# Kernel tuning notes

Measured on AMD Instinct MI355X. Metric: run time of the kernel, lower is better.

## Reference

```python
import jax, jax.numpy as jnp
import numpy as np

B, T, NC, NB, D, DH = 128, 200, 3, 2, 512, 256
IMG_W, IMG_H = 640.0, 400.0


def setup_inputs() -> dict:
    key = jax.random.key(0)
    ks = jax.random.split(key, 16)
    # box_data: [x1,y1,x2,y2,category,confidence], some boxes zeroed (missing)
    coords = jax.random.uniform(ks[0], (B, T, NC * NB, 4)) * jnp.array([IMG_W, IMG_H, IMG_W, IMG_H])
    keep = (jax.random.uniform(ks[1], (B, T, NC * NB, 1)) > 0.2).astype(jnp.float32)
    coords = coords * keep
    cat = jax.random.randint(ks[2], (B, T, NC * NB, 1), 0, 3).astype(jnp.float32)
    conf = jax.random.uniform(ks[3], (B, T, NC * NB, 1))
    box_data = jnp.concatenate([coords, cat, conf], axis=-1)
    w = lambda k, shape: jax.random.normal(k, shape, jnp.float32) * 0.02
    return {
        "box_data": box_data,
        "cat_table": w(ks[4], (3, D)),
        "geom_w1": w(ks[5], (10, DH)), "geom_b1": jnp.zeros((DH,), jnp.float32),
        "ln_g": jnp.ones((DH,), jnp.float32), "ln_b": jnp.zeros((DH,), jnp.float32),
        "geom_w2": w(ks[6], (DH, D)), "geom_b2": jnp.zeros((D,), jnp.float32),
        "conf_w": w(ks[7], (1, D)), "conf_b": jnp.zeros((D,), jnp.float32),
        "center_w": w(ks[8], (2, D)), "center_b": jnp.zeros((D,), jnp.float32),
        "missing_emb": w(ks[9], (1, D)),
        "dist_w": w(ks[10], (1, D)), "dist_b": jnp.zeros((D,), jnp.float32),
        "cam_table": w(ks[11], (NC, D)),
        "scale": jnp.float32(3.0),
    }


def _layernorm(x, g, b, eps=1e-5):
    mu = jnp.mean(x, axis=-1, keepdims=True)
    var = jnp.mean(jnp.square(x - mu), axis=-1, keepdims=True)
    return (x - mu) * jax.lax.rsqrt(var + eps) * g + b


def reference(box_data, cat_table, geom_w1, geom_b1, ln_g, ln_b, geom_w2, geom_b2,
              conf_w, conf_b, center_w, center_b, missing_emb, dist_w, dist_b,
              cam_table, scale):
    coords = box_data[..., :4]                                 # (B,T,6,4)
    category = box_data[..., 4].astype(jnp.int32)
    conf = box_data[..., 5]
    norm = jnp.array([IMG_W, IMG_H, IMG_W, IMG_H], box_data.dtype)
    cn = (coords / norm).reshape(B, T, NC, NB, 4)              # normalized coords
    category = category.reshape(B, T, NC, NB)
    conf = conf.reshape(B, T, NC, NB, 1)
    presence = (cn.sum(-1) != 0).astype(box_data.dtype)        # (B,T,NC,NB)
    # sort boxes within each camera by category, missing boxes last
    sort_key = category.astype(box_data.dtype) + (1.0 - presence) * 1000.0
    idx = jnp.argsort(sort_key, axis=-1)                       # (B,T,NC,NB)
    cn = jnp.take_along_axis(cn, idx[..., None], axis=-2)
    category = jnp.take_along_axis(category, idx, axis=-1)
    conf = jnp.take_along_axis(conf, idx[..., None], axis=-2)
    presence = (cn.sum(-1) != 0).astype(box_data.dtype)[..., None]  # (B,T,NC,NB,1)

    x1, y1, x2, y2 = cn[..., 0], cn[..., 1], cn[..., 2], cn[..., 3]
    width, height = x2 - x1, y2 - y1
    cx, cy = (x1 + x2) * 0.5, (y1 + y2) * 0.5
    area = width * height
    aspect = width / (height + 1e-6)

    # distance token per camera (between the 2 boxes)
    dx, dy = cx[..., 0] - cx[..., 1], cy[..., 0] - cy[..., 1]
    dist = jnp.sqrt(dx * dx + dy * dy)[..., None]              # (B,T,NC,1)
    dist_tok = dist @ dist_w + dist_b                          # (B,T,NC,D)
    dist_flat = dist_tok.reshape(B, T * NC, D)

    geom = jnp.stack([x1, y1, x2, y2, width, height, cx, cy, area, aspect], axis=-1)
    h = _layernorm(geom @ geom_w1 + geom_b1, ln_g, ln_b)
    h = jax.nn.gelu(h, approximate=False)                      # torch GELU is exact
    geom_p = h @ geom_w2 + geom_b2                             # (B,T,NC,NB,D)

    cat_emb = cat_table[category]                              # (B,T,NC,NB,D)
    conf_p = conf @ conf_w + conf_b
    center_p = jnp.stack([cx, cy], axis=-1) @ center_w + center_b
    cam_emb = cam_table.reshape(1, 1, NC, 1, D)

    tok = (geom_p + cat_emb + conf_p + center_p + cam_emb) * scale
    tok = jnp.where(presence == 0, missing_emb, tok)           # (1,D) broadcasts
    tok_flat = tok.reshape(B, T * NC * NB, D)
    return jnp.concatenate([dist_flat, tok_flat], axis=1)      # (B, T*NC*(1+NB), D)
```

## Files before the change

### kernel.cpp

```cpp
#include <hip/hip_runtime.h>
#include <hip/hip_bf16.h>
#include <cstdint>

constexpr int Bn = 128, Tn = 200, NCn = 3, NBn = 2, Dn = 512, DHn = 256;
constexpr int GROUPS = Bn * Tn * NCn;
constexpr int TOKS   = GROUPS * NBn;

typedef __bf16 bf16x8 __attribute__((ext_vector_type(8)));
typedef float  f32x4  __attribute__((ext_vector_type(4)));

__device__ __forceinline__ unsigned short f2b(float f) {
    union { float f; unsigned int u; } x; x.f = f;
    unsigned int r = x.u + 0x7fffu + ((x.u >> 16) & 1u);
    return (unsigned short)(r >> 16);
}

__device__ __forceinline__ f32x4 ld4(const float* __restrict__ p) {
    return *reinterpret_cast<const f32x4*>(p);
}

__global__ __launch_bounds__(256) void k_tr(const float* __restrict__ w2,
                                            unsigned short* __restrict__ w2t) {
    int idx = blockIdx.x * 256 + threadIdx.x;
    int n = idx >> 8, k = idx & 255;
    w2t[idx] = f2b(w2[k * Dn + n]);
}

__global__ __launch_bounds__(256) void k_main(
    const float* __restrict__ bd,
    const float* __restrict__ cat_table,
    const float* __restrict__ w1,
    const float* __restrict__ b1,
    const float* __restrict__ ln_g,
    const float* __restrict__ ln_b,
    const float* __restrict__ b2v,
    const float* __restrict__ conf_w,
    const float* __restrict__ conf_b,
    const float* __restrict__ center_w,
    const float* __restrict__ center_b,
    const float* __restrict__ missing,
    const float* __restrict__ cam_table,
    const float* __restrict__ scale_p,
    const float* __restrict__ dist_w,
    const float* __restrict__ dist_b,
    const unsigned short* __restrict__ w2t,
    float* __restrict__ out) {

    __shared__ float s_geom[64][12];
    __shared__ float s_scal[64][4];
    __shared__ unsigned short s_a[64 * 264];

    const int tid = threadIdx.x;
    const int tb  = blockIdx.x * 64;

    if (tid < 32) {
        int g = blockIdx.x * 32 + tid;
        const float* p = bd + (size_t)g * 12;
        float v[12];
        #pragma unroll
        for (int i = 0; i < 12; i++) v[i] = p[i];
        float cn[2][4];
        cn[0][0] = v[0] / 640.f; cn[0][1] = v[1] / 400.f; cn[0][2] = v[2] / 640.f; cn[0][3] = v[3] / 400.f;
        cn[1][0] = v[6] / 640.f; cn[1][1] = v[7] / 400.f; cn[1][2] = v[8] / 640.f; cn[1][3] = v[9] / 400.f;
        float catv[2] = { v[4], v[10] };
        float cnfv[2] = { v[5], v[11] };
        float sum0 = cn[0][0] + cn[0][1] + cn[0][2] + cn[0][3];
        float sum1 = cn[1][0] + cn[1][1] + cn[1][2] + cn[1][3];
        float pr0 = (sum0 != 0.f) ? 1.f : 0.f;
        float pr1 = (sum1 != 0.f) ? 1.f : 0.f;
        float key0 = catv[0] + (1.f - pr0) * 1000.f;
        float key1 = catv[1] + (1.f - pr1) * 1000.f;
        int sw = (key1 < key0) ? 1 : 0;
        #pragma unroll
        for (int s = 0; s < 2; s++) {
            int src = s ^ sw;
            float x1 = cn[src][0], y1 = cn[src][1], x2 = cn[src][2], y2 = cn[src][3];
            float wd = x2 - x1, ht = y2 - y1;
            float cx = (x1 + x2) * 0.5f, cy = (y1 + y2) * 0.5f;
            float area = wd * ht, asp = wd / (ht + 1e-6f);
            float pres = ((x1 + y1 + x2 + y2) != 0.f) ? 1.f : 0.f;
            int lt = tid * 2 + s;
            s_geom[lt][0] = x1; s_geom[lt][1] = y1; s_geom[lt][2] = x2; s_geom[lt][3] = y2;
            s_geom[lt][4] = wd; s_geom[lt][5] = ht; s_geom[lt][6] = cx; s_geom[lt][7] = cy;
            s_geom[lt][8] = area; s_geom[lt][9] = asp; s_geom[lt][10] = 0.f; s_geom[lt][11] = 0.f;
            s_scal[lt][0] = cnfv[src]; s_scal[lt][1] = cx; s_scal[lt][2] = cy;
            s_scal[lt][3] = catv[src] + ((pres == 0.f) ? 4.f : 0.f);
        }
    }
    __syncthreads();

    const int w = tid >> 6, lane = tid & 63;

    {
        const int c0 = lane * 4;
        f32x4 w1r[10], b1r, gr, br;
        #pragma unroll
        for (int f = 0; f < 10; f++) w1r[f] = ld4(w1 + f * DHn + c0);
        b1r = ld4(b1 + c0); gr = ld4(ln_g + c0); br = ld4(ln_b + c0);
        for (int i = 0; i < 16; i++) {
            int lt = w * 16 + i;
            float gm[10];
            #pragma unroll
            for (int f = 0; f < 10; f++) gm[f] = s_geom[lt][f];
            float x[4];
            #pragma unroll
            for (int qq = 0; qq < 4; qq++) {
                float a = b1r[qq];
                #pragma unroll
                for (int f = 0; f < 10; f++) a += gm[f] * w1r[f][qq];
                x[qq] = a;
            }
            float s  = x[0] + x[1] + x[2] + x[3];
            float s2 = x[0]*x[0] + x[1]*x[1] + x[2]*x[2] + x[3]*x[3];
            #pragma unroll
            for (int m = 1; m < 64; m <<= 1) {
                s  += __shfl_xor(s,  m, 64);
                s2 += __shfl_xor(s2, m, 64);
            }
            float mu  = s * (1.f / 256.f);
            float var = s2 * (1.f / 256.f) - mu * mu;
            float rstd = rsqrtf(var + 1e-5f);
            ushort4 pk;
            #pragma unroll
            for (int qq = 0; qq < 4; qq++) {
                float t = (x[qq] - mu) * rstd * gr[qq] + br[qq];
                float y = 0.5f * t * (1.f + erff(t * 0.70710678118f));
                ((unsigned short*)&pk)[qq] = f2b(y);
            }
            *reinterpret_cast<ushort4*>(&s_a[lt * 264 + c0]) = pk;
        }
    }
    __syncthreads();

    const int mtp = w & 1;
    const int nh  = w >> 1;
    const int r16 = lane & 15, q = lane >> 4;

    bf16x8 afr[2][8];
    #pragma unroll
    for (int mt = 0; mt < 2; mt++) {
        int row = (mtp * 2 + mt) * 16 + r16;
        const unsigned short* base = &s_a[row * 264 + q * 8];
        #pragma unroll
        for (int ks = 0; ks < 8; ks++)
            afr[mt][ks] = *reinterpret_cast<const bf16x8*>(base + ks * 32);
    }

    float rconf[8], rcx[8], rcy[8];
    int rcat[8], rcam[8];
    size_t rowoff[8];
    bool rpres[8];
    #pragma unroll
    for (int i = 0; i < 8; i++) {
        int mt = i >> 2, r = i & 3;
        int m = (mtp * 2 + mt) * 16 + q * 4 + r;
        rconf[i] = s_scal[m][0]; rcx[i] = s_scal[m][1]; rcy[i] = s_scal[m][2];
        int code = (int)s_scal[m][3];
        rcat[i] = code & 3; rpres[i] = (code < 4);
        int gt = tb + m;
        rcam[i] = (gt >> 1) % 3;
        int b = gt / 1200, rr = gt - b * 1200;
        rowoff[i] = ((size_t)b * 1800 + 600 + rr) * Dn;
    }
    float sc = scale_p[0];

    for (int ntl = 0; ntl < 16; ntl++) {
        int n = (nh * 16 + ntl) * 16 + r16;
        float cb  = b2v[n] + conf_b[n] + center_b[n];
        float cwv = conf_w[n];
        float c0v = center_w[n];
        float c1v = center_w[Dn + n];
        float msv = missing[n];

        f32x4 acc0 = {0.f, 0.f, 0.f, 0.f}, acc1 = {0.f, 0.f, 0.f, 0.f};
        const unsigned short* bbase = w2t + n * 256 + q * 8;
        #pragma unroll
        for (int ks = 0; ks < 8; ks++) {
            bf16x8 bf = *reinterpret_cast<const bf16x8*>(bbase + ks * 32);
            acc0 = __builtin_amdgcn_mfma_f32_16x16x32_bf16(afr[0][ks], bf, acc0, 0, 0, 0);
            acc1 = __builtin_amdgcn_mfma_f32_16x16x32_bf16(afr[1][ks], bf, acc1, 0, 0, 0);
        }
        #pragma unroll
        for (int i = 0; i < 8; i++) {
            int mt = i >> 2, r = i & 3;
            float a = (mt == 0) ? acc0[r] : acc1[r];
            float ce = cat_table[rcat[i] * Dn + n];
            float cm = cam_table[rcam[i] * Dn + n];
            float v = (a + cb + ce + rconf[i] * cwv + rcx[i] * c0v + rcy[i] * c1v + cm) * sc;
            if (!rpres[i]) v = msv;
            out[rowoff[i] + n] = v;
        }
    }

    {
        const int gl2 = tid >> 7;
        const int col = (tid & 127) * 4;
        const f32x4 dwv = ld4(dist_w + col);
        const f32x4 dbv = ld4(dist_b + col);
        const int gblk = blockIdx.x * 32;
        for (int p = 0; p < 16; ++p) {
            int gl = p * 2 + gl2;
            float dx = s_scal[2 * gl][1] - s_scal[2 * gl + 1][1];
            float dy = s_scal[2 * gl][2] - s_scal[2 * gl + 1][2];
            float dist = sqrtf(dx * dx + dy * dy);
            int g = gblk + gl;
            int b = g / 600, r = g - b * 600;
            size_t ro = ((size_t)b * 1800 + r) * Dn + col;
            f32x4 v;
            #pragma unroll
            for (int r4 = 0; r4 < 4; r4++) v[r4] = dist * dwv[r4] + dbv[r4];
            *reinterpret_cast<f32x4*>(out + ro) = v;
        }
    }
}

extern "C" void kernel_launch(void* const* d_in, const int* in_sizes, int n_in,
                              void* d_out, int out_size, void* d_ws, size_t ws_size,
                              hipStream_t stream) {
    const float* bd        = (const float*)d_in[0];
    const float* cat_table = (const float*)d_in[1];
    const float* w1        = (const float*)d_in[2];
    const float* b1        = (const float*)d_in[3];
    const float* ln_g      = (const float*)d_in[4];
    const float* ln_b      = (const float*)d_in[5];
    const float* w2        = (const float*)d_in[6];
    const float* b2v       = (const float*)d_in[7];
    const float* conf_w    = (const float*)d_in[8];
    const float* conf_b    = (const float*)d_in[9];
    const float* center_w  = (const float*)d_in[10];
    const float* center_b  = (const float*)d_in[11];
    const float* missing   = (const float*)d_in[12];
    const float* dist_w    = (const float*)d_in[13];
    const float* dist_b    = (const float*)d_in[14];
    const float* cam_table = (const float*)d_in[15];
    const float* scale_p   = (const float*)d_in[16];
    float* out = (float*)d_out;
    unsigned short* w2t = (unsigned short*)d_ws;

    hipLaunchKernelGGL(k_tr, dim3(512), dim3(256), 0, stream, w2, w2t);
    hipLaunchKernelGGL(k_main, dim3(TOKS / 64), dim3(256), 0, stream,
                       bd, cat_table, w1, b1, ln_g, ln_b, b2v, conf_w, conf_b,
                       center_w, center_b, missing, cam_table, scale_p,
                       dist_w, dist_b, w2t, out);
}
```

Measured before the change: 674.7 us.

## Fold bias, embedding and missing-token terms into augmented MFMA K dimension

Extends the GEMM reduction from 256 to 288 by appending per-token feature columns to the activation tile and matching columns to the transposed weights. The extra columns are presence, conf, cx, cy, one-hot category, one-hot camera and a not-present flag; the weights hold the bias sum, conf/center weights, category and camera tables, and missing/scale. This removes the per-element gathers of cat_table, cam_table and several bias vectors, plus the select, from the epilogue, which becomes a single scale and store. In exchange it adds one more MFMA k-step per tile and stores those additive terms in bf16, which loses some precision.

Result: slower. 698.8 us (+3.6%).

```diff
diff --git a/kernel.cpp b/kernel.cpp
--- a/kernel.cpp
+++ b/kernel.cpp
@@ -5,6 +5,8 @@
 constexpr int Bn = 128, Tn = 200, NCn = 3, NBn = 2, Dn = 512, DHn = 256;
 constexpr int GROUPS = Bn * Tn * NCn;
 constexpr int TOKS   = GROUPS * NBn;
+constexpr int KE = 288;
+constexpr int SA_STRIDE = 296;
 
 typedef __bf16 bf16x8 __attribute__((ext_vector_type(8)));
 typedef float  f32x4  __attribute__((ext_vector_type(4)));
@@ -19,27 +21,43 @@
     return *reinterpret_cast<const f32x4*>(p);
 }
 
-__global__ __launch_bounds__(256) void k_tr(const float* __restrict__ w2,
-                                            unsigned short* __restrict__ w2t) {
-    int idx = blockIdx.x * 256 + threadIdx.x;
-    int n = idx >> 8, k = idx & 255;
-    w2t[idx] = f2b(w2[k * Dn + n]);
+__global__ __launch_bounds__(256) void k_tr(
+    const float* __restrict__ w2,
+    const float* __restrict__ b2v,
+    const float* __restrict__ conf_b,
+    const float* __restrict__ center_b,
+    const float* __restrict__ conf_w,
+    const float* __restrict__ center_w,
+    const float* __restrict__ cat_table,
+    const float* __restrict__ cam_table,
+    const float* __restrict__ missing,
+    const float* __restrict__ scale_p,
+    unsigned short* __restrict__ w2t) {
+    int n = blockIdx.x;
+    int k = threadIdx.x;
+    w2t[n * KE + k] = f2b(w2[k * Dn + n]);
+    if (k < 32) {
+        float v = 0.f;
+        switch (k) {
+            case 0: v = b2v[n] + conf_b[n] + center_b[n]; break;
+            case 1: v = conf_w[n]; break;
+            case 2: v = center_w[n]; break;
+            case 3: v = center_w[Dn + n]; break;
+            case 4: case 5: case 6: v = cat_table[(k - 4) * Dn + n]; break;
+            case 7: case 8: case 9: v = cam_table[(k - 7) * Dn + n]; break;
+            case 10: v = missing[n] / scale_p[0]; break;
+            default: break;
+        }
+        w2t[n * KE + 256 + k] = f2b(v);
+    }
 }
 
 __global__ __launch_bounds__(256) void k_main(
     const float* __restrict__ bd,
-    const float* __restrict__ cat_table,
     const float* __restrict__ w1,
     const float* __restrict__ b1,
     const float* __restrict__ ln_g,
     const float* __restrict__ ln_b,
-    const float* __restrict__ b2v,
-    const float* __restrict__ conf_w,
-    const float* __restrict__ conf_b,
-    const float* __restrict__ center_w,
-    const float* __restrict__ center_b,
-    const float* __restrict__ missing,
-    const float* __restrict__ cam_table,
     const float* __restrict__ scale_p,
     const float* __restrict__ dist_w,
     const float* __restrict__ dist_b,
@@ -48,7 +66,7 @@
 
     __shared__ float s_geom[64][12];
     __shared__ float s_scal[64][4];
-    __shared__ unsigned short s_a[64 * 264];
+    __shared__ unsigned short s_a[64 * SA_STRIDE];
 
     const int tid = threadIdx.x;
     const int tb  = blockIdx.x * 64;
@@ -92,6 +110,34 @@
     const int w = tid >> 6, lane = tid & 63;
 
     {
+        int tok = tid >> 2, grp = tid & 3;
+        float cf = s_scal[tok][0], cx = s_scal[tok][1], cy = s_scal[tok][2];
+        int code = (int)s_scal[tok][3];
+        int cat = code & 3;
+        float prs = (code < 4) ? 1.f : 0.f;
+        int gt = tb + tok;
+        int cam = (gt >> 1) % 3;
+        unsigned short pk[8];
+        #pragma unroll
+        for (int j = 0; j < 8; j++) {
+            int e = grp * 8 + j;
+            float v = 0.f;
+            if (e == 0) v = prs;
+            else if (e == 1) v = cf * prs;
+            else if (e == 2) v = cx * prs;
+            else if (e == 3) v = cy * prs;
+            else if (e >= 4 && e < 7)  v = (e - 4 == cat) ? prs : 0.f;
+            else if (e >= 7 && e < 10) v = (e - 7 == cam) ? prs : 0.f;
+            else if (e == 10) v = 1.f - prs;
+            pk[j] = f2b(v);
+        }
+        *reinterpret_cast<ushort4*>(&s_a[tok * SA_STRIDE + 256 + grp * 8])
+            = *reinterpret_cast<ushort4*>(&pk[0]);
+        *reinterpret_cast<ushort4*>(&s_a[tok * SA_STRIDE + 260 + grp * 8])
+            = *reinterpret_cast<ushort4*>(&pk[4]);
+    }
+
+    {
         const int c0 = lane * 4;
         f32x4 w1r[10], b1r, gr, br;
         #pragma unroll
@@ -102,6 +148,7 @@
             float gm[10];
             #pragma unroll
             for (int f = 0; f < 10; f++) gm[f] = s_geom[lt][f];
+            float prs = (s_scal[lt][3] < 3.5f) ? 1.f : 0.f;
             float x[4];
             #pragma unroll
             for (int qq = 0; qq < 4; qq++) {
@@ -120,14 +167,14 @@
             float mu  = s * (1.f / 256.f);
             float var = s2 * (1.f / 256.f) - mu * mu;
             float rstd = rsqrtf(var + 1e-5f);
-            ushort4 pk;
+            ushort4 pkv;
             #pragma unroll
             for (int qq = 0; qq < 4; qq++) {
                 float t = (x[qq] - mu) * rstd * gr[qq] + br[qq];
-                float y = 0.5f * t * (1.f + erff(t * 0.70710678118f));
-                ((unsigned short*)&pk)[qq] = f2b(y);
+                float y = 0.5f * t * (1.f + erff(t * 0.70710678118f)) * prs;
+                ((unsigned short*)&pkv)[qq] = f2b(y);
             }
-            *reinterpret_cast<ushort4*>(&s_a[lt * 264 + c0]) = pk;
+            *reinterpret_cast<ushort4*>(&s_a[lt * SA_STRIDE + c0]) = pkv;
         }
     }
     __syncthreads();
@@ -136,46 +183,33 @@
     const int nh  = w >> 1;
     const int r16 = lane & 15, q = lane >> 4;
 
-    bf16x8 afr[2][8];
+    bf16x8 afr[2][9];
     #pragma unroll
     for (int mt = 0; mt < 2; mt++) {
         int row = (mtp * 2 + mt) * 16 + r16;
-        const unsigned short* base = &s_a[row * 264 + q * 8];
-        #pragma unroll
-        for (int ks = 0; ks < 8; ks++)
+        const unsigned short* base = &s_a[row * SA_STRIDE + q * 8];
+        #pragma unroll
+        for (int ks = 0; ks < 9; ks++)
             afr[mt][ks] = *reinterpret_cast<const bf16x8*>(base + ks * 32);
     }
 
-    float rconf[8], rcx[8], rcy[8];
-    int rcat[8], rcam[8];
-    size_t rowoff[8];
-    bool rpres[8];
+    unsigned int rowoff[8];
     #pragma unroll
     for (int i = 0; i < 8; i++) {
         int mt = i >> 2, r = i & 3;
         int m = (mtp * 2 + mt) * 16 + q * 4 + r;
-        rconf[i] = s_scal[m][0]; rcx[i] = s_scal[m][1]; rcy[i] = s_scal[m][2];
-        int code = (int)s_scal[m][3];
-        rcat[i] = code & 3; rpres[i] = (code < 4);
         int gt = tb + m;
-        rcam[i] = (gt >> 1) % 3;
         int b = gt / 1200, rr = gt - b * 1200;
-        rowoff[i] = ((size_t)b * 1800 + 600 + rr) * Dn;
-    }
-    float sc = scale_p[0];
+        rowoff[i] = ((unsigned int)b * 1800u + 600u + (unsigned int)rr) * (unsigned int)Dn;
+    }
+    const float sc = scale_p[0];
 
     for (int ntl = 0; ntl < 16; ntl++) {
         int n = (nh * 16 + ntl) * 16 + r16;
-        float cb  = b2v[n] + conf_b[n] + center_b[n];
-        float cwv = conf_w[n];
-        float c0v = center_w[n];
-        float c1v = center_w[Dn + n];
-        float msv = missing[n];
-
         f32x4 acc0 = {0.f, 0.f, 0.f, 0.f}, acc1 = {0.f, 0.f, 0.f, 0.f};
-        const unsigned short* bbase = w2t + n * 256 + q * 8;
-        #pragma unroll
-        for (int ks = 0; ks < 8; ks++) {
+        const unsigned short* bbase = w2t + (size_t)n * KE + q * 8;
+        #pragma unroll
+        for (int ks = 0; ks < 9; ks++) {
             bf16x8 bf = *reinterpret_cast<const bf16x8*>(bbase + ks * 32);
             acc0 = __builtin_amdgcn_mfma_f32_16x16x32_bf16(afr[0][ks], bf, acc0, 0, 0, 0);
             acc1 = __builtin_amdgcn_mfma_f32_16x16x32_bf16(afr[1][ks], bf, acc1, 0, 0, 0);
@@ -184,11 +218,7 @@
         for (int i = 0; i < 8; i++) {
             int mt = i >> 2, r = i & 3;
             float a = (mt == 0) ? acc0[r] : acc1[r];
-            float ce = cat_table[rcat[i] * Dn + n];
-            float cm = cam_table[rcam[i] * Dn + n];
-            float v = (a + cb + ce + rconf[i] * cwv + rcx[i] * c0v + rcy[i] * c1v + cm) * sc;
-            if (!rpres[i]) v = msv;
-            out[rowoff[i] + n] = v;
+            out[(size_t)rowoff[i] + n] = a * sc;
         }
     }
 
@@ -237,9 +267,9 @@
     float* out = (float*)d_out;
     unsigned short* w2t = (unsigned short*)d_ws;
 
-    hipLaunchKernelGGL(k_tr, dim3(512), dim3(256), 0, stream, w2, w2t);
+    hipLaunchKernelGGL(k_tr, dim3(512), dim3(256), 0, stream,
+                       w2, b2v, conf_b, center_b, conf_w, center_w,
+                       cat_table, cam_table, missing, scale_p, w2t);
     hipLaunchKernelGGL(k_main, dim3(TOKS / 64), dim3(256), 0, stream,
-                       bd, cat_table, w1, b1, ln_g, ln_b, b2v, conf_w, conf_b,
-                       center_w, center_b, missing, cam_table, scale_p,
-                       dist_w, dist_b, w2t, out);
-}
+                       bd, w1, b1, ln_g, ln_b, scale_p, dist_w, dist_b, w2t, out);
+}
```
